# Kernel tuning notes

Measured on AMD Instinct MI355X. Metric: run time of the kernel, lower is better.

## Reference

```python
import jax, jax.numpy as jnp
import numpy as np

N, EG, T, H, EC, L, NT = 10000, 200000, 300000, 128, 128, 3, 100


def _ssp(x):
    # ShiftedSoftplus: softplus(x) - log(2)
    return jax.nn.softplus(x) - jnp.log(2.0).astype(x.dtype)


def _bn(x, g, b):
    # BatchNorm1d in training mode: biased batch stats, eps=1e-5
    m = jnp.mean(x, axis=0)
    v = jnp.var(x, axis=0)
    return g * (x - m) * jax.lax.rsqrt(v + 1e-5) + b


def _forward(z, i, j, idx_i, idx_j, idx_k, idx_ji, idx_kj, pos,
             We1, be1, We2, be2, We3, be3,
             Wc1, bc1, g_c1, b_c1, g_n, b_n,
             Wc2, bc2, g_c2, b_c2, Wc3, bc3, g_c3, b_c3,
             g_c22, b_c22, g_c32, b_c32,
             Wf1, bf1, Wf2, bf2, Wf3, bf3):
    # AtomType2NodeEmb
    h = jax.nn.one_hot(z, NT, dtype=jnp.float32)
    h = _ssp(h @ We1 + be1)
    h = _ssp(h @ We2 + be2)
    node = h @ We3 + be3                      # [N, H]
    # geometry + GaussianFilter edge embedding
    rel = pos[i] - pos[j]                     # [EG, 3]
    dist = jnp.sqrt(jnp.sum(rel * rel, axis=-1))
    unit = rel / dist[:, None]
    offset = jnp.linspace(0.0, 5.0, EC)
    coeff = -0.5 / (offset[1] - offset[0]) ** 2
    edge = jnp.exp(coeff * (dist[:, None] - offset[None, :]) ** 2)  # [EG, EC]
    for l in range(L):
        # NodeUpdate
        c1 = jnp.concatenate([node[i], edge], axis=1) @ Wc1[l] + bc1[l]
        c1 = _bn(c1, g_c1[l], b_c1[l])
        f1, r1 = jnp.split(c1, 2, axis=1)
        agg = jax.ops.segment_sum(jax.nn.sigmoid(f1) * jnp.tanh(r1), i, num_segments=N)
        node = jnp.tanh(node + _bn(agg, g_n[l], b_n[l]))
        # EdgeUpdate: pair term
        c2 = (node[i] * node[j]) @ Wc2[l] + bc2[l]
        c2 = _bn(c2, g_c2[l], b_c2[l])
        f2, r2 = jnp.split(c2, 2, axis=1)
        c2_emb = _bn(jax.nn.sigmoid(f2) * jnp.tanh(r2), g_c22[l], b_c22[l])
        # EdgeUpdate: triplet term
        c3 = jnp.concatenate([node[idx_i], node[idx_j], node[idx_k],
                              edge[idx_ji], edge[idx_kj]], axis=1) @ Wc3[l] + bc3[l]
        c3 = _bn(c3, g_c3[l], b_c3[l])
        f3, r3 = jnp.split(c3, 2, axis=1)
        agg3 = jax.ops.segment_sum(jax.nn.sigmoid(f3) * jnp.tanh(r3), idx_ji, num_segments=EG)
        c3_emb = _bn(agg3, g_c32[l], b_c32[l])
        edge = jnp.tanh(edge + c2_emb + c3_emb)
    # ForcePredictor
    f = _ssp(edge @ Wf1 + bf1)
    f = _ssp(f @ Wf2 + bf2)
    force = (f @ Wf3 + bf3) * unit            # [EG, 3]
    return jax.ops.segment_sum(force, i, num_segments=N)


def setup_inputs() -> dict:
    ks = iter(jax.random.split(jax.random.key(0), 32))

    def w(shape):
        return jax.random.normal(next(ks), shape, jnp.float32) * (shape[-2] ** -0.5)

    z = jax.random.randint(next(ks), (N,), 0, NT)
    pos = jax.random.uniform(next(ks), (N, 3), jnp.float32) * 5.0
    i = jax.random.randint(next(ks), (EG,), 0, N)
    j = (i + 1 + jax.random.randint(next(ks), (EG,), 0, N - 1)) % N  # no self-loops
    idx_i = jax.random.randint(next(ks), (T,), 0, N)
    idx_j = jax.random.randint(next(ks), (T,), 0, N)
    idx_k = jax.random.randint(next(ks), (T,), 0, N)
    idx_ji = jax.random.randint(next(ks), (T,), 0, EG)
    idx_kj = jax.random.randint(next(ks), (T,), 0, EG)
    return dict(
        z=z, pos=pos, i=i, j=j, idx_i=idx_i, idx_j=idx_j, idx_k=idx_k,
        idx_ji=idx_ji, idx_kj=idx_kj,
        We1=w((NT, H)), be1=jnp.zeros((H,)), We2=w((H, H)), be2=jnp.zeros((H,)),
        We3=w((H, H)), be3=jnp.zeros((H,)),
        Wc1=w((L, H + EC, 2 * H)), bc1=jnp.zeros((L, 2 * H)),
        g_c1=jnp.ones((L, 2 * H)), b_c1=jnp.zeros((L, 2 * H)),
        g_n=jnp.ones((L, H)), b_n=jnp.zeros((L, H)),
        Wc2=w((L, H, 2 * EC)), bc2=jnp.zeros((L, 2 * EC)),
        g_c2=jnp.ones((L, 2 * EC)), b_c2=jnp.zeros((L, 2 * EC)),
        Wc3=w((L, 3 * H + 2 * EC, 2 * EC)), bc3=jnp.zeros((L, 2 * EC)),
        g_c3=jnp.ones((L, 2 * EC)), b_c3=jnp.zeros((L, 2 * EC)),
        g_c22=jnp.ones((L, EC)), b_c22=jnp.zeros((L, EC)),
        g_c32=jnp.ones((L, EC)), b_c32=jnp.zeros((L, EC)),
        Wf1=w((EC, EC)), bf1=jnp.zeros((EC,)), Wf2=w((EC, EC)), bf2=jnp.zeros((EC,)),
        Wf3=w((EC, 1)), bf3=jnp.zeros((1,)),
    )


def reference(z, pos, i, j, idx_i, idx_j, idx_k, idx_ji, idx_kj,
              We1, be1, We2, be2, We3, be3,
              Wc1, bc1, g_c1, b_c1, g_n, b_n,
              Wc2, bc2, g_c2, b_c2, Wc3, bc3, g_c3, b_c3,
              g_c22, b_c22, g_c32, b_c32,
              Wf1, bf1, Wf2, bf2, Wf3, bf3):
    return _forward(z, i, j, idx_i, idx_j, idx_k, idx_ji, idx_kj, pos,
                    We1, be1, We2, be2, We3, be3,
                    Wc1, bc1, g_c1, b_c1, g_n, b_n,
                    Wc2, bc2, g_c2, b_c2, Wc3, bc3, g_c3, b_c3,
                    g_c22, b_c22, g_c32, b_c32,
                    Wf1, bf1, Wf2, bf2, Wf3, bf3)
```

## Files before the change

kernel.cpp:

```cpp
#include <hip/hip_runtime.h>

typedef unsigned short u16;
typedef unsigned int   u32;
typedef __attribute__((ext_vector_type(8))) short short8;
typedef __attribute__((ext_vector_type(4))) float f32x4;

#define NN  10000
#define EGN 200000
#define TTN 300000
#define LLN 3

__device__ __forceinline__ float b2f(u16 u){ union{u32 i; float f;} x; x.i=(u32)u<<16; return x.f; }
__device__ __forceinline__ u16 f2b(float f){ union{float f; u32 u;} x; x.f=f; u32 r=(x.u + 0x7fffu + ((x.u>>16)&1u))>>16; return (u16)r; }
__device__ __forceinline__ float sigf(float x){ return 1.f/(1.f+__expf(-x)); }
__device__ __forceinline__ float tanhf_(float x){ float e=__expf(2.f*x); return 1.f - 2.f/(e+1.f); }
__device__ __forceinline__ float sspf(float x){ return fmaxf(x,0.f) + log1pf(__expf(-fabsf(x))) - 0.6931471805599453f; }

__device__ __forceinline__ void async16(void* lds, const void* g){
  __builtin_amdgcn_global_load_lds((const __attribute__((address_space(1))) void*)g,
                                   (__attribute__((address_space(3))) void*)lds, 16, 0, 0);
}
__device__ __forceinline__ void split_store(float v, u16* ph, u16* pl, size_t o){
  u16 h = f2b(v); ph[o] = h; pl[o] = f2b(v - b2f(h));
}
__device__ __forceinline__ short8 ldfrag(const u16* P, int row, int kk, int lane){
  int kg = kk*4 + (lane>>4);
  int slot = kg ^ (row&7);
  return *(const short8*)(P + row*64 + slot*8);
}

struct Segs {
  const u16* sh[10];
  const u16* sl[10];
  const int* idx[10];
  int coff[10];
};

template<int NP, int ROWS>
__device__ __forceinline__ void stageA(u16* Ah, u16* Al,
    const u16* sh, const u16* sl, const int* idxp, int coff,
    int rb, int M, int tid){
#pragma unroll
  for (int rnd=0; rnd<ROWS/32; ++rnd){
    int u = rnd*256 + tid;
    int row = u>>3, s = u&7, sw = s ^ (row&7);
    int grow = rb + row; if (grow >= M) grow = M-1;
    int srow = idxp ? idxp[grow] : grow;
    size_t go = (size_t)srow*256 + coff + sw*16;
    async16(Ah + u*8, (const char*)sh + go);
    if (NP==2) async16(Al + u*8, (const char*)sl + go);
  }
}

template<int NP, int ROWS>
__device__ __forceinline__ void stageA_prod(u16* Ah, u16* Al,
    const u16* nh, const u16* nl, const int* pii, const int* pjj,
    int rb, int M, int ks, int tid){
#pragma unroll
  for (int rep=0; rep<ROWS/64; ++rep){
    int row = rep*64 + (tid>>2), q = tid&3;
    int e = rb + row; if (e >= M) e = M-1;
    int ia = pii[e], ja = pjj[e];
    const u16* phi = nh + (size_t)ia*128 + ks*64 + q*16;
    const u16* pli = nl + (size_t)ia*128 + ks*64 + q*16;
    const u16* phj = nh + (size_t)ja*128 + ks*64 + q*16;
    const u16* plj = nl + (size_t)ja*128 + ks*64 + q*16;
#pragma unroll
    for (int c=0;c<2;c++){
      short8 hi = *(const short8*)(phi + c*8);
      short8 li = *(const short8*)(pli + c*8);
      short8 hj = *(const short8*)(phj + c*8);
      short8 lj = *(const short8*)(plj + c*8);
      short8 vh, vl;
#pragma unroll
      for (int k=0;k<8;k++){
        float a = b2f((u16)hi[k]) + b2f((u16)li[k]);
        float b = b2f((u16)hj[k]) + b2f((u16)lj[k]);
        float v = a*b;
        u16 h = f2b(v);
        vh[k] = (short)h;
        vl[k] = (short)f2b(v - b2f(h));
      }
      int g = q*2 + c, slot = g ^ (row&7);
      *(short8*)(Ah + row*64 + slot*8) = vh;
      if (NP==2) *(short8*)(Al + row*64 + slot*8) = vl;
    }
  }
}

// ... 55 lines not shown
    for (int kk=0;kk<2;kk++){
      short8 a[4];
#pragma unroll
      for (int m=0;m<4;m++) a[m] = ldfrag(Ah, m*16 + lane15, kk, lane);
#pragma unroll
      for (int n=0;n<4;n++){
        short8 b = ldfrag(Bh, wv*64 + n*16 + lane15, kk, lane);
#pragma unroll
        for (int m=0;m<4;m++)
          acc[m][n] = __builtin_amdgcn_mfma_f32_16x16x32_bf16(a[m], b, acc[m][n], 0,0,0);
      }
    }
    __syncthreads();
  }
#pragma unroll
  for (int n=0;n<4;n++){
    int col = wv*64 + n*16 + lane15;
    float bb = bias[col];
    float s=0.f, q=0.f;
#pragma unroll
    for (int m=0;m<4;m++){
#pragma unroll
      for (int r=0;r<4;r++){
        int grow = rb + m*16 + (lane>>4)*4 + r;
        if (grow < M){ float v = acc[m][n][r] + bb; s += v; q += v*v; }
      }
    }
    s += __shfl_xor(s,16); s += __shfl_xor(s,32);
    q += __shfl_xor(q,16); q += __shfl_xor(q,32);
    if (lane < 16){ atomicAdd(&ls[wv*64 + n*16 + lane], s); atomicAdd(&lq[wv*64 + n*16 + lane], q); }
  }
  __syncthreads();
  atomicAdd(&st[tid], ls[tid]); atomicAdd(&st[256+tid], lq[tid]);
}

template<int NP, bool PROD, int EPI>
__global__ __launch_bounds__(256) void gemm_pair(
  int M, int nseg, Segs segs,
  const u16* __restrict__ nh, const u16* __restrict__ nl,
  const int* __restrict__ pii, const int* __restrict__ pjj,
  const u16* __restrict__ Wh, const u16* __restrict__ Wl, int K2b,
  const float* __restrict__ bias,
  const float* __restrict__ st, const float* __restrict__ g, const float* __restrict__ b, float inv,
  const int* __restrict__ sidx, float* __restrict__ aggout,
  const float* __restrict__ st22, const float* __restrict__ g22, const float* __restrict__ b22,
  const float* __restrict__ st32, const float* __restrict__ g32, const float* __restrict__ b32, float inv2,
  const float* __restrict__ agg3, u16* __restrict__ eh, u16* __restrict__ el,
  float* __restrict__ st22out)
{
  __shared__ u16 Ah[64*64];
  __shared__ u16 Al[NP==2 ? 64*64 : 64];
  __shared__ u16 Bh[128*64];
  __shared__ u16 Bl[NP==2 ? 128*64 : 64];
  __shared__ float ls[64], lq[64];
  __shared__ float sAf[64], sCf[64], sAr[64], sCr[64];
  __shared__ float sA22[64], sC22[64], sA32[64], sC32[64];
  const int tid = threadIdx.x, lane = tid&63, wv = tid>>6;
  const int lane15 = lane&15;
  const int rb = blockIdx.x*64, P0 = blockIdx.y*64;

  if (tid < 64){
    int p = P0 + tid;
    float m1 = st[p]*inv,     v1 = st[256+p]*inv - m1*m1;
    float a1 = g[p]*rsqrtf(v1+1e-5f);
    sAf[tid]=a1; sCf[tid]=b[p]-a1*m1;
    float m2 = st[128+p]*inv, v2 = st[384+p]*inv - m2*m2;
    float a2 = g[128+p]*rsqrtf(v2+1e-5f);
    sAr[tid]=a2; sCr[tid]=b[128+p]-a2*m2;
    if (EPI==1){
      float m3 = st22[p]*inv2, v3 = st22[128+p]*inv2 - m3*m3;
      float a3 = g22[p]*rsqrtf(v3+1e-5f);
      sA22[tid]=a3; sC22[tid]=b22[p]-a3*m3;
      float m4 = st32[p]*inv2, v4 = st32[128+p]*inv2 - m4*m4;
      float a4 = g32[p]*rsqrtf(v4+1e-5f);
      sA32[tid]=a4; sC32[tid]=b32[p]-a4*m4;
    }
    if (EPI==2){ ls[tid]=0.f; lq[tid]=0.f; }
  }

  f32x4 accf[4], accr[4];
#pragma unroll
  for (int m=0;m<4;m++){ accf[m]=(f32x4){0.f,0.f,0.f,0.f}; accr[m]=(f32x4){0.f,0.f,0.f,0.f}; }

  for (int ks=0; ks<nseg; ++ks){
    if (PROD) stageA_prod<NP,64>(Ah, Al, nh, nl, pii, pjj, rb, M, ks, tid);
    else      stageA<NP,64>(Ah, Al, segs.sh[ks], segs.sl[ks], segs.idx[ks], segs.coff[ks], rb, M, tid);
    stageB_pair<NP>(Bh, Bl, Wh, Wl, P0, K2b, ks*128, tid);
    __syncthreads();
#pragma unroll
    for (int kk=0;kk<2;kk++){
      short8 ah[4], al[4];
#pragma unroll
      for (int m=0;m<4;m++){
        ah[m] = ldfrag(Ah, m*16 + lane15, kk, lane);
        if constexpr (NP==2) al[m] = ldfrag(Al, m*16 + lane15, kk, lane);
      }
      short8 bfh = ldfrag(Bh, wv*16 + lane15,      kk, lane);
      short8 brh = ldfrag(Bh, 64 + wv*16 + lane15, kk, lane);
      short8 bfl, brl;
      if constexpr (NP==2){
        bfl = ldfrag(Bl, wv*16 + lane15,      kk, lane);
        brl = ldfrag(Bl, 64 + wv*16 + lane15, kk, lane);
      }
#pragma unroll
      for (int m=0;m<4;m++){
        accf[m] = __builtin_amdgcn_mfma_f32_16x16x32_bf16(ah[m], bfh, accf[m], 0,0,0);
        accr[m] = __builtin_amdgcn_mfma_f32_16x16x32_bf16(ah[m], brh, accr[m], 0,0,0);
        if constexpr (NP==2){
          accf[m] = __builtin_amdgcn_mfma_f32_16x16x32_bf16(ah[m], bfl, accf[m], 0,0,0);
          accf[m] = __builtin_amdgcn_mfma_f32_16x16x32_bf16(al[m], bfh, accf[m], 0,0,0);
          accr[m] = __builtin_amdgcn_mfma_f32_16x16x32_bf16(ah[m], brl, accr[m], 0,0,0);
          accr[m] = __builtin_amdgcn_mfma_f32_16x16x32_bf16(al[m], brh, accr[m], 0,0,0);
        }
      }
    }
    __syncthreads();
  }

  const int pp = wv*16 + lane15;
  const int p  = P0 + pp;
  const float bf_ = bias[p], br_ = bias[128+p];
  const float Af = sAf[pp], Cf = sCf[pp], Ar = sAr[pp], Cr = sCr[pp];
  float su=0.f, sq=0.f;
#pragma unroll
  for (int m=0;m<4;m++){
#pragma unroll
    for (int r=0;r<4;r++){
      int grow = rb + m*16 + (lane>>4)*4 + r;
      if (grow >= M) continue;
      float yf = accf[m][r] + bf_;
      float yr = accr[m][r] + br_;
      float u = sigf(Af*yf + Cf) * tanhf_(Ar*yr + Cr);
      if (EPI==0){
        atomicAdd(&aggout[(size_t)sidx[grow]*128 + p], u);
      } else if (EPI==1){
        size_t o = (size_t)grow*128 + p;
        float eo = b2f(eh[o]) + b2f(el[o]);
        float v = tanhf_(eo + sA22[pp]*u + sC22[pp] + sA32[pp]*agg3[o] + sC32[pp]);
        split_store(v, eh, el, o);
      } else {
        su += u; sq += u*u;
      }
    }
  }
  if (EPI==2){
    su += __shfl_xor(su,16); su += __shfl_xor(su,32);
    sq += __shfl_xor(sq,16); sq += __shfl_xor(sq,32);
    if (lane < 16){ atomicAdd(&ls[wv*16+lane], su); atomicAdd(&lq[wv*16+lane], sq); }
    __syncthreads();
    if (tid < 64){ atomicAdd(&st22out[P0+tid], ls[tid]); atomicAdd(&st22out[128+P0+tid], lq[tid]); }
  }
}

__global__ __launch_bounds__(256) void gemm_force(
  int M, Segs segs,
  const u16* __restrict__ Wh, const u16* __restrict__ Wl, int K2b,
  const float* __restrict__ bias, u16* __restrict__ oh, u16* __restrict__ ol)
{
  __shared__ u16 Ah[64*64], Al[64*64];
  __shared__ u16 Bh[128*64], Bl[128*64];
  const int tid = threadIdx.x, lane = tid&63, wv = tid>>6;
  const int lane15 = lane&15;
  const int rb = blockIdx.x*64;

  f32x4 acc[4][2];
#pragma unroll
  for (int m=0;m<4;m++)
#pragma unroll
    for (int n=0;n<2;n++) acc[m][n] = (f32x4){0.f,0.f,0.f,0.f};

  for (int ks=0; ks<2; ++ks){
    stageA<2,64>(Ah, Al, segs.sh[ks], segs.sl[ks], segs.idx[ks], segs.coff[ks], rb, M, tid);
    stageB_id<2,128>(Bh, Bl, Wh, Wl, K2b, ks*128, tid);
    __syncthreads();
#pragma unroll
    for (int kk=0;kk<2;kk++){
      short8 ah[4], al[4];
#pragma unroll
      for (int m=0;m<4;m++){
        ah[m] = ldfrag(Ah, m*16 + lane15, kk, lane);
        al[m] = ldfrag(Al, m*16 + lane15, kk, lane);
      }
#pragma unroll
      for (int n=0;n<2;n++){
        short8 bh = ldfrag(Bh, wv*32 + n*16 + lane15, kk, lane);
        short8 bl = ldfrag(Bl, wv*32 + n*16 + lane15, kk, lane);
#pragma unroll
        for (int m=0;m<4;m++){
          acc[m][n] = __builtin_amdgcn_mfma_f32_16x16x32_bf16(ah[m], bh, acc[m][n], 0,0,0);
          acc[m][n] = __builtin_amdgcn_mfma_f32_16x16x32_bf16(ah[m], bl, acc[m][n], 0,0,0);
          acc[m][n] = __builtin_amdgcn_mfma_f32_16x16x32_bf16(al[m], bh, acc[m][n], 0,0,0);
        }
      }
    }
    __syncthreads();
  }
#pragma unroll
  for (int n=0;n<2;n++){
    int col = wv*32 + n*16 + lane15;
    float bb = bias[col];
#pragma unroll
    for (int m=0;m<4;m++){
#pragma unroll
      for (int r=0;r<4;r++){
        int grow = rb + m*16 + (lane>>4)*4 + r;
        if (grow < M){
          float v = sspf(acc[m][n][r] + bb);
          split_store(v, oh, ol, (size_t)grow*128 + col);
        }
      }
    }
  }
}

__global__ void transpose_cvt(const float* __restrict__ src, u16* __restrict__ dh, u16* __restrict__ dl, int K, int N){
  __shared__ float t[32][33];
  const float* s = src + (size_t)blockIdx.z * K * N;
  u16* dsth = dh + (size_t)blockIdx.z * K * N;
  u16* dstl = dl + (size_t)blockIdx.z * K * N;
  int n0 = blockIdx.x*32, k0 = blockIdx.y*32;
  for (int dy=threadIdx.y; dy<32; dy+=8){
    int k = k0+dy, n = n0+threadIdx.x;
    if (k<K && n<N) t[dy][threadIdx.x] = s[(size_t)k*N + n];
  }
  __syncthreads();
  for (int dy=threadIdx.y; dy<32; dy+=8){
    int n = n0+dy, k = k0+threadIdx.x;
    if (n<N && k<K) split_store(t[threadIdx.x][dy], dsth, dstl, (size_t)n*K + k);
  }
}

__global__ __launch_bounds__(128) void embed_k(const int* __restrict__ z,
  const float* __restrict__ We1, const float* __restrict__ be1,
  const float* __restrict__ We2, const float* __restrict__ be2,
  const float* __restrict__ We3, const float* __restrict__ be3,
  u16* __restrict__ nh, u16* __restrict__ nl){
  __shared__ float h0[128], h1[128];
  int nid = blockIdx.x, t = threadIdx.x;
  int zz = z[nid];
  h0[t] = sspf(We1[zz*128 + t] + be1[t]);
  __syncthreads();
  float a = be2[t];
  for (int k=0;k<128;k++) a += h0[k]*We2[k*128+t];
  h1[t] = sspf(a);
  __syncthreads();
  float b = be3[t];
  for (int k=0;k<128;k++) b += h1[k]*We3[k*128+t];
  split_store(b, nh, nl, (size_t)nid*128+t);
}

__global__ __launch_bounds__(256) void geom_k(const float* __restrict__ pos,
  const int* __restrict__ ii, const int* __restrict__ jj,
  float* __restrict__ unitv, u16* __restrict__ eh, u16* __restrict__ el){
  int t = threadIdx.x; int e = blockIdx.x*2 + (t>>7); int col = t&127;
  int a = ii[e], b = jj[e];
  float dx = pos[a*3]-pos[b*3], dy=pos[a*3+1]-pos[b*3+1], dz=pos[a*3+2]-pos[b*3+2];
  float dist = sqrtf(dx*dx+dy*dy+dz*dz);
  if (col==0){ float inv=1.f/dist; unitv[e*3]=dx*inv; unitv[e*3+1]=dy*inv; unitv[e*3+2]=dz*inv; }
  const float step = 5.0f/127.0f;
  const float coeff = -0.5f/(step*step);
  float d = dist - step*(float)col;
  float g = __expf(coeff*d*d);
  split_store(g, eh, el, (size_t)e*128+col);
}

__global__ __launch_bounds__(256) void colstats128(const float* __restrict__ m, int M, float* __restrict__ st){
  __shared__ float ls[128], lq[128];
  int t=threadIdx.x; if(t<128){ls[t]=0.f;lq[t]=0.f;} __syncthreads();
  int col=t&127, hf=t>>7; float ps=0.f,pq=0.f;
  int npair=(M+1)>>1;
  for (int pr=blockIdx.x; pr<npair; pr+=gridDim.x){
    int row=pr*2+hf;
    if(row<M){ float v=m[(size_t)row*128+col]; ps+=v; pq+=v*v; }
  }
  atomicAdd(&ls[col],ps); atomicAdd(&lq[col],pq);
  __syncthreads();
  if(t<128){ atomicAdd(&st[t],ls[t]); atomicAdd(&st[128+t],lq[t]); }
}

__global__ __launch_bounds__(256) void node_update_k(u16* __restrict__ nh, u16* __restrict__ nl,
  const float* __restrict__ agg, const float* __restrict__ st,
  const float* __restrict__ g, const float* __restrict__ b, float inv, int Nn)
{
  int t=threadIdx.x; int col=t&127, hf=t>>7;
  float mean = st[col]*inv;
  float var  = st[128+col]*inv - mean*mean;
  float A = g[col]*rsqrtf(var+1e-5f);
  float C = b[col] - A*mean;
  int npair=(Nn+1)>>1;
  for (int pr=blockIdx.x; pr<npair; pr+=gridDim.x){
    int row=pr*2+hf; if(row>=Nn) continue;
    size_t o=(size_t)row*128+col;
    float nv = b2f(nh[o]) + b2f(nl[o]);
    float v = tanhf_(nv + A*agg[o] + C);
    split_store(v, nh, nl, o);
  }
}

__global__ __launch_bounds__(256) void force_k(const u16* __restrict__ fh, const u16* __restrict__ fl,
  const float* __restrict__ Wf3, const float* __restrict__ bf3,
  const float* __restrict__ unitv, const int* __restrict__ ii, float* __restrict__ outp, int Me)
{
  int wv=threadIdx.x>>6, lane=threadIdx.x&63;
  int e = blockIdx.x*4 + wv; if(e>=Me) return;
  size_t o0=(size_t)e*128+lane, o1=o0+64;
  float p = (b2f(fh[o0])+b2f(fl[o0]))*Wf3[lane] + (b2f(fh[o1])+b2f(fl[o1]))*Wf3[64+lane];
  for (int s=32;s>0;s>>=1) p += __shfl_down(p, s);
  if (lane==0){
    float F = p + bf3[0];
    atomicAdd(&outp[ii[e]*3+0], F*unitv[e*3+0]);
    atomicAdd(&outp[ii[e]*3+1], F*unitv[e*3+1]);
    atomicAdd(&outp[ii[e]*3+2], F*unitv[e*3+2]);
  }
}

__global__ void sentinel_k(float* o, int n, float v){
  int i = blockIdx.x*256 + threadIdx.x; if (i<n) o[i]=v;
}

extern "C" void kernel_launch(void* const* d_in, const int* in_sizes, int n_in,
                              void* d_out, int out_size, void* d_ws, size_t ws_size,
                              hipStream_t stream)
{
  (void)in_sizes; (void)n_in;
  const int* z      = (const int*)d_in[0];
  const float* pos  = (const float*)d_in[1];
  const int* ii     = (const int*)d_in[2];
  const int* jj     = (const int*)d_in[3];
  const int* idx_i  = (const int*)d_in[4];
  const int* idx_j  = (const int*)d_in[5];
  const int* idx_k  = (const int*)d_in[6];
  const int* idx_ji = (const int*)d_in[7];
  const int* idx_kj = (const int*)d_in[8];
  const float* We1=(const float*)d_in[9];  const float* be1=(const float*)d_in[10];
  const float* We2=(const float*)d_in[11]; const float* be2=(const float*)d_in[12];
  const float* We3=(const float*)d_in[13]; const float* be3=(const float*)d_in[14];
  const float* Wc1=(const float*)d_in[15]; const float* bc1=(const float*)d_in[16];
  const float* g_c1=(const float*)d_in[17]; const float* b_c1=(const float*)d_in[18];
  const float* g_n=(const float*)d_in[19]; const float* b_n=(const float*)d_in[20];
  const float* Wc2=(const float*)d_in[21]; const float* bc2=(const float*)d_in[22];
  const float* g_c2=(const float*)d_in[23]; const float* b_c2=(const float*)d_in[24];
  const float* Wc3=(const float*)d_in[25]; const float* bc3=(const float*)d_in[26];
  const float* g_c3=(const float*)d_in[27]; const float* b_c3=(const float*)d_in[28];
  const float* g_c22=(const float*)d_in[29]; const float* b_c22=(const float*)d_in[30];
  const float* g_c32=(const float*)d_in[31]; const float* b_c32=(const float*)d_in[32];
  const float* Wf1=(const float*)d_in[33]; const float* bf1=(const float*)d_in[34];
  const float* Wf2=(const float*)d_in[35]; const float* bf2=(const float*)d_in[36];
  const float* Wf3=(const float*)d_in[37]; const float* bf3=(const float*)d_in[38];

  char* ws = (char*)d_ws;
  size_t off=0;
  auto alloc=[&](size_t bb){ size_t o=off; off += (bb+255)&~(size_t)255; return o; };
  u16*   node_h = (u16*)(ws + alloc((size_t)NN*128*2));
  u16*   node_l = (u16*)(ws + alloc((size_t)NN*128*2));
  u16*   edge_h = (u16*)(ws + alloc((size_t)EGN*128*2));
  u16*   edge_l = (u16*)(ws + alloc((size_t)EGN*128*2));
  float* unitv  = (float*)(ws + alloc((size_t)EGN*3*4));
  float* agg    = (float*)(ws + alloc((size_t)NN*128*4));
  float* agg3   = (float*)(ws + alloc((size_t)EGN*128*4));
  u16*   wc1h   = (u16*)(ws + alloc((size_t)3*256*256*2));
  u16*   wc1l   = (u16*)(ws + alloc((size_t)3*256*256*2));
  u16*   wc2h   = (u16*)(ws + alloc((size_t)3*256*128*2));
  u16*   wc2l   = (u16*)(ws + alloc((size_t)3*256*128*2));
  u16*   wc3h   = (u16*)(ws + alloc((size_t)3*256*640*2));
  u16*   wc3l   = (u16*)(ws + alloc((size_t)3*256*640*2));
  u16*   wf1h   = (u16*)(ws + alloc((size_t)128*128*2));
  u16*   wf1l   = (u16*)(ws + alloc((size_t)128*128*2));
  u16*   wf2h   = (u16*)(ws + alloc((size_t)128*128*2));
  u16*   wf2l   = (u16*)(ws + alloc((size_t)128*128*2));
  float* stats  = (float*)(ws + alloc(2304*4));

  if (off > ws_size){
    sentinel_k<<<(out_size+255)/256, 256, 0, stream>>>((float*)d_out, out_size, 123456.0f);
    return;
  }

  float* st1 = stats;
  float* st2 = stats+512;
  float* st3 = stats+1024;
  float* stN = stats+1536;
  float* st32= stats+1792;
  float* st22= stats+2048;

  u16* f1h = (u16*)agg3;
  u16* f1l = f1h + (size_t)EGN*128;
  u16* f2h = edge_h;
  u16* f2l = edge_l;

  hipMemsetAsync(d_out, 0, (size_t)out_size*4, stream);

  dim3 tb(32,8);
  transpose_cvt<<<dim3(8,8,3),  tb, 0, stream>>>(Wc1, wc1h, wc1l, 256, 256);
  transpose_cvt<<<dim3(8,4,3),  tb, 0, stream>>>(Wc2, wc2h, wc2l, 128, 256);
  transpose_cvt<<<dim3(8,20,3), tb, 0, stream>>>(Wc3, wc3h, wc3l, 640, 256);
  transpose_cvt<<<dim3(4,4,1),  tb, 0, stream>>>(Wf1, wf1h, wf1l, 128, 128);
  transpose_cvt<<<dim3(4,4,1),  tb, 0, stream>>>(Wf2, wf2h, wf2l, 128, 128);

  embed_k<<<NN,128,0,stream>>>(z, We1,be1,We2,be2,We3,be3, node_h, node_l);
  geom_k<<<EGN/2,256,0,stream>>>(pos, ii, jj, unitv, edge_h, edge_l);

  const int gE64  = (EGN+63)/64;
  const int gT64  = (TTN+63)/64;
  Segs dummy{};
  const float invE = 1.0f/EGN, invT = 1.0f/TTN, invN = 1.0f/NN;

  for (int l=0;l<LLN;l++){
    hipMemsetAsync(stats, 0, 2304*4, stream);
    hipMemsetAsync(agg,  0, (size_t)NN*128*4, stream);
    hipMemsetAsync(agg3, 0, (size_t)EGN*128*4, stream);

    const u16* w1h = wc1h + l*256*256; const u16* w1l = wc1l + l*256*256;
    const u16* w2h = wc2h + l*256*128; const u16* w2l = wc2l + l*256*128;
    const u16* w3h = wc3h + l*256*640; const u16* w3l = wc3l + l*256*640;

    Segs s1{};
    s1.sh[0]=node_h; s1.sl[0]=node_l; s1.idx[0]=ii;      s1.coff[0]=0;
    s1.sh[1]=node_h; s1.sl[1]=node_l; s1.idx[1]=ii;      s1.coff[1]=128;
    s1.sh[2]=edge_h; s1.sl[2]=edge_l; s1.idx[2]=nullptr; s1.coff[2]=0;
    s1.sh[3]=edge_h; s1.sl[3]=edge_l; s1.idx[3]=nullptr; s1.coff[3]=128;
    gemm_stats<false><<<gE64,256,0,stream>>>(EGN, 4, s1, nullptr,nullptr,nullptr,nullptr,
                                             w1h, 512, bc1+l*256, st1);
    gemm_pair<2,false,0><<<dim3(gE64,2),256,0,stream>>>(EGN, 4, s1, nullptr,nullptr,nullptr,nullptr,
        w1h, w1l, 512, bc1+l*256,
        st1, g_c1+l*256, b_c1+l*256, invE,
        ii, agg,
        nullptr,nullptr,nullptr, nullptr,nullptr,nullptr, 0.f,
        nullptr, nullptr, nullptr, nullptr);
    colstats128<<<256,256,0,stream>>>(agg, NN, stN);
    node_update_k<<<2048,256,0,stream>>>(node_h, node_l, agg, stN, g_n+l*128, b_n+l*128, invN, NN);

    Segs s3{};
    s3.sh[0]=node_h; s3.sl[0]=node_l; s3.idx[0]=idx_i;  s3.coff[0]=0;
    s3.sh[1]=node_h; s3.sl[1]=node_l; s3.idx[1]=idx_i;  s3.coff[1]=128;
    s3.sh[2]=node_h; s3.sl[2]=node_l; s3.idx[2]=idx_j;  s3.coff[2]=0;
    s3.sh[3]=node_h; s3.sl[3]=node_l; s3.idx[3]=idx_j;  s3.coff[3]=128;
    s3.sh[4]=node_h; s3.sl[4]=node_l; s3.idx[4]=idx_k;  s3.coff[4]=0;
    s3.sh[5]=node_h; s3.sl[5]=node_l; s3.idx[5]=idx_k;  s3.coff[5]=128;
    s3.sh[6]=edge_h; s3.sl[6]=edge_l; s3.idx[6]=idx_ji; s3.coff[6]=0;
    s3.sh[7]=edge_h; s3.sl[7]=edge_l; s3.idx[7]=idx_ji; s3.coff[7]=128;
    s3.sh[8]=edge_h; s3.sl[8]=edge_l; s3.idx[8]=idx_kj; s3.coff[8]=0;
    s3.sh[9]=edge_h; s3.sl[9]=edge_l; s3.idx[9]=idx_kj; s3.coff[9]=128;
    gemm_stats<false><<<gT64,256,0,stream>>>(TTN, 10, s3, nullptr,nullptr,nullptr,nullptr,
                                             w3h, 1280, bc3+l*256, st3);
    gemm_pair<2,false,0><<<dim3(gT64,2),256,0,stream>>>(TTN, 10, s3, nullptr,nullptr,nullptr,nullptr,
        w3h, w3l, 1280, bc3+l*256,
        st3, g_c3+l*256, b_c3+l*256, invT,
        idx_ji, agg3,
        nullptr,nullptr,nullptr, nullptr,nullptr,nullptr, 0.f,
        nullptr, nullptr, nullptr, nullptr);
    colstats128<<<1024,256,0,stream>>>(agg3, EGN, st32);

    gemm_stats<true><<<gE64,256,0,stream>>>(EGN, 2, dummy, node_h,node_l,ii,jj,
                                            w2h, 256, bc2+l*256, st2);
    gemm_pair<1,true,2><<<dim3(gE64,2),256,0,stream>>>(EGN, 2, dummy, node_h,node_l,ii,jj,
        w2h, nullptr, 256, bc2+l*256,
        st2, g_c2+l*256, b_c2+l*256, invE,
        nullptr, nullptr,
        nullptr,nullptr,nullptr, nullptr,nullptr,nullptr, 0.f,
        nullptr, nullptr, nullptr, st22);
    gemm_pair<2,true,1><<<dim3(gE64,2),256,0,stream>>>(EGN, 2, dummy, node_h,node_l,ii,jj,
        w2h, w2l, 256, bc2+l*256,
        st2, g_c2+l*256, b_c2+l*256, invE,
        nullptr, nullptr,
        st22, g_c22+l*128, b_c22+l*128, st32, g_c32+l*128, b_c32+l*128, invE,
        agg3, edge_h, edge_l, nullptr);
  }

  Segs sf1{}; sf1.sh[0]=edge_h; sf1.sl[0]=edge_l; sf1.idx[0]=nullptr; sf1.coff[0]=0;
              sf1.sh[1]=edge_h; sf1.sl[1]=edge_l; sf1.idx[1]=nullptr; sf1.coff[1]=128;
  gemm_force<<<gE64,256,0,stream>>>(EGN, sf1, wf1h, wf1l, 256, bf1, f1h, f1l);
  Segs sf2{}; sf2.sh[0]=f1h; sf2.sl[0]=f1l; sf2.idx[0]=nullptr; sf2.coff[0]=0;
              sf2.sh[1]=f1h; sf2.sl[1]=f1l; sf2.idx[1]=nullptr; sf2.coff[1]=128;
  gemm_force<<<gE64,256,0,stream>>>(EGN, sf2, wf2h, wf2l, 256, bf2, f2h, f2l);
  force_k<<<(EGN+3)/4,256,0,stream>>>(f2h, f2l, Wf3, bf3, unitv, ii, (float*)d_out, EGN);
}
```

Before: 4.164 ms.

## Sort edges and triplets by scatter key and coalesce segment-sum atomics

Adds a per-call counting sort (histogram, scan, rank, permute) that reorders edges by source node and triplets by their remapped target edge. All edge state is stored in sorted order and the triplet indices are remapped to match. The EPI==0 epilogue then accumulates consecutive rows that share a segment id in registers and issues one atomic per run instead of one per row. This is meant to cut global atomic traffic and improve gather locality, at the cost of about twenty extra small launches and nondeterministic ordering within each segment from the atomic-based ranking.

```diff
diff --git a/kernel.cpp b/kernel.cpp
--- a/kernel.cpp
+++ b/kernel.cpp
@@ -35,6 +35,61 @@
   const int* idx[10];
   int coff[10];
 };
+
+__global__ void hist_k(const int* __restrict__ keys, int n, int* __restrict__ hist){
+  int i = blockIdx.x*256 + threadIdx.x;
+  if (i<n) atomicAdd(&hist[keys[i]], 1);
+}
+__global__ __launch_bounds__(256) void scan_tile_k(const int* __restrict__ in, int n,
+                                                   int* __restrict__ out, int* __restrict__ tilesum){
+  __shared__ int ts[256];
+  int b=blockIdx.x, t=threadIdx.x;
+  int base=b*2048+t*8;
+  int v[8], s=0;
+#pragma unroll
+  for(int k=0;k<8;k++){ int i=base+k; v[k]=(i<n)?in[i]:0; s+=v[k]; }
+  ts[t]=s; __syncthreads();
+  if(t==0){ int acc=0; for(int k=0;k<256;k++){int x=ts[k]; ts[k]=acc; acc+=x;} tilesum[b]=acc; }
+  __syncthreads();
+  int acc=ts[t];
+#pragma unroll
+  for(int k=0;k<8;k++){ int i=base+k; if(i<n) out[i]=acc; acc+=v[k]; }
+}
+__global__ void scan_sum_k(int* tilesum, int ntiles){
+  if(threadIdx.x==0 && blockIdx.x==0){
+    int acc=0; for(int k=0;k<ntiles;k++){int x=tilesum[k]; tilesum[k]=acc; acc+=x;}
+  }
+}
+__global__ __launch_bounds__(256) void scan_add_k(int* __restrict__ out, int n, const int* __restrict__ tilesum){
+  int i=blockIdx.x*256+threadIdx.x; if(i<n) out[i] += tilesum[i>>11];
+}
+__global__ void rank_k(const int* __restrict__ keys, int n, const int* __restrict__ basearr,
+                       int* __restrict__ cnt, int* __restrict__ rank){
+  int i=blockIdx.x*256+threadIdx.x; if(i>=n) return;
+  int k=keys[i];
+  rank[i] = basearr[k] + atomicAdd(&cnt[k],1);
+}
+__global__ void remap2_k(const int* __restrict__ a, const int* __restrict__ b,
+                         const int* __restrict__ table, int n,
+                         int* __restrict__ oa, int* __restrict__ ob){
+  int i=blockIdx.x*256+threadIdx.x; if(i>=n) return;
+  oa[i]=table[a[i]]; ob[i]=table[b[i]];
+}
+__global__ void permute2_k(const int* __restrict__ rank, int n,
+                           const int* __restrict__ a, const int* __restrict__ b,
+                           int* __restrict__ pa, int* __restrict__ pb){
+  int i=blockIdx.x*256+threadIdx.x; if(i>=n) return;
+  int r=rank[i]; pa[r]=a[i]; pb[r]=b[i];
+}
+__global__ void permute5_k(const int* __restrict__ rank, int n,
+                           const int* __restrict__ a, const int* __restrict__ b, const int* __restrict__ c,
+                           const int* __restrict__ d, const int* __restrict__ e,
+                           int* __restrict__ pa, int* __restrict__ pb, int* __restrict__ pc,
+                           int* __restrict__ pd, int* __restrict__ pe){
+  int i=blockIdx.x*256+threadIdx.x; if(i>=n) return;
+  int r=rank[i];
+  pa[r]=a[i]; pb[r]=b[i]; pc[r]=c[i]; pd[r]=d[i]; pe[r]=e[i];
+}
 
 template<int NP, int ROWS>
 __device__ __forceinline__ void stageA(u16* Ah, u16* Al,
@@ -265,34 +320,55 @@
   const int p  = P0 + pp;
   const float bf_ = bias[p], br_ = bias[128+p];
   const float Af = sAf[pp], Cf = sCf[pp], Ar = sAr[pp], Cr = sCr[pp];
-  float su=0.f, sq=0.f;
-#pragma unroll
-  for (int m=0;m<4;m++){
-#pragma unroll
-    for (int r=0;r<4;r++){
-      int grow = rb + m*16 + (lane>>4)*4 + r;
-      if (grow >= M) continue;
-      float yf = accf[m][r] + bf_;
-      float yr = accr[m][r] + br_;
-      float u = sigf(Af*yf + Cf) * tanhf_(Ar*yr + Cr);
-      if (EPI==0){
-        atomicAdd(&aggout[(size_t)sidx[grow]*128 + p], u);
-      } else if (EPI==1){
-        size_t o = (size_t)grow*128 + p;
-        float eo = b2f(eh[o]) + b2f(el[o]);
-        float v = tanhf_(eo + sA22[pp]*u + sC22[pp] + sA32[pp]*agg3[o] + sC32[pp]);
-        split_store(v, eh, el, o);
-      } else {
-        su += u; sq += u*u;
-      }
-    }
-  }
-  if (EPI==2){
-    su += __shfl_xor(su,16); su += __shfl_xor(su,32);
-    sq += __shfl_xor(sq,16); sq += __shfl_xor(sq,32);
-    if (lane < 16){ atomicAdd(&ls[wv*16+lane], su); atomicAdd(&lq[wv*16+lane], sq); }
-    __syncthreads();
-    if (tid < 64){ atomicAdd(&st22out[P0+tid], ls[tid]); atomicAdd(&st22out[128+P0+tid], lq[tid]); }
+
+  if constexpr (EPI==0){
+    int cur = -1; float run = 0.f;
+#pragma unroll
+    for (int m=0;m<4;m++){
+#pragma unroll
+      for (int r=0;r<4;r++){
+        int grow = rb + m*16 + (lane>>4)*4 + r;
+        if (grow >= M) continue;
+        float yf = accf[m][r] + bf_;
+        float yr = accr[m][r] + br_;
+        float u = sigf(Af*yf + Cf) * tanhf_(Ar*yr + Cr);
+        int sv = sidx[grow];
+        if (sv != cur){
+          if (cur >= 0) atomicAdd(&aggout[(size_t)cur*128 + p], run);
+          cur = sv; run = 0.f;
+        }
+        run += u;
+      }
+    }
+    if (cur >= 0) atomicAdd(&aggout[(size_t)cur*128 + p], run);
+  } else {
+    float su=0.f, sq=0.f;
+#pragma unroll
+    for (int m=0;m<4;m++){
+#pragma unroll
+      for (int r=0;r<4;r++){
+        int grow = rb + m*16 + (lane>>4)*4 + r;
+        if (grow >= M) continue;
+        float yf = accf[m][r] + bf_;
+        float yr = accr[m][r] + br_;
+        float u = sigf(Af*yf + Cf) * tanhf_(Ar*yr + Cr);
+        if (EPI==1){
+          size_t o = (size_t)grow*128 + p;
+          float eo = b2f(eh[o]) + b2f(el[o]);
+          float v = tanhf_(eo + sA22[pp]*u + sC22[pp] + sA32[pp]*agg3[o] + sC32[pp]);
+          split_store(v, eh, el, o);
+        } else {
+          su += u; sq += u*u;
+        }
+      }
+    }
+    if (EPI==2){
+      su += __shfl_xor(su,16); su += __shfl_xor(su,32);
+      sq += __shfl_xor(sq,16); sq += __shfl_xor(sq,32);
+      if (lane < 16){ atomicAdd(&ls[wv*16+lane], su); atomicAdd(&lq[wv*16+lane], sq); }
+      __syncthreads();
+      if (tid < 64){ atomicAdd(&st22out[P0+tid], ls[tid]); atomicAdd(&st22out[128+P0+tid], lq[tid]); }
+    }
   }
 }
 
@@ -394,18 +470,19 @@
 }
 
 __global__ __launch_bounds__(256) void geom_k(const float* __restrict__ pos,
-  const int* __restrict__ ii, const int* __restrict__ jj,
+  const int* __restrict__ ii, const int* __restrict__ jj, const int* __restrict__ ranke,
   float* __restrict__ unitv, u16* __restrict__ eh, u16* __restrict__ el){
   int t = threadIdx.x; int e = blockIdx.x*2 + (t>>7); int col = t&127;
   int a = ii[e], b = jj[e];
+  int r = ranke[e];
   float dx = pos[a*3]-pos[b*3], dy=pos[a*3+1]-pos[b*3+1], dz=pos[a*3+2]-pos[b*3+2];
   float dist = sqrtf(dx*dx+dy*dy+dz*dz);
-  if (col==0){ float inv=1.f/dist; unitv[e*3]=dx*inv; unitv[e*3+1]=dy*inv; unitv[e*3+2]=dz*inv; }
+  if (col==0){ float inv=1.f/dist; unitv[r*3]=dx*inv; unitv[r*3+1]=dy*inv; unitv[r*3+2]=dz*inv; }
   const float step = 5.0f/127.0f;
   const float coeff = -0.5f/(step*step);
   float d = dist - step*(float)col;
   float g = __expf(coeff*d*d);
-  split_store(g, eh, el, (size_t)e*128+col);
+  split_store(g, eh, el, (size_t)r*128+col);
 }
 
 __global__ __launch_bounds__(256) void colstats128(const float* __restrict__ m, int M, float* __restrict__ st){
@@ -443,7 +520,7 @@
 
 __global__ __launch_bounds__(256) void force_k(const u16* __restrict__ fh, const u16* __restrict__ fl,
   const float* __restrict__ Wf3, const float* __restrict__ bf3,
-  const float* __restrict__ unitv, const int* __restrict__ ii, float* __restrict__ outp, int Me)
+  const float* __restrict__ unitv, const int* __restrict__ pii, float* __restrict__ outp, int Me)
 {
   int wv=threadIdx.x>>6, lane=threadIdx.x&63;
   int e = blockIdx.x*4 + wv; if(e>=Me) return;
@@ -452,9 +529,9 @@
   for (int s=32;s>0;s>>=1) p += __shfl_down(p, s);
   if (lane==0){
     float F = p + bf3[0];
-    atomicAdd(&outp[ii[e]*3+0], F*unitv[e*3+0]);
-    atomicAdd(&outp[ii[e]*3+1], F*unitv[e*3+1]);
-    atomicAdd(&outp[ii[e]*3+2], F*unitv[e*3+2]);
+    atomicAdd(&outp[pii[e]*3+0], F*unitv[e*3+0]);
+    atomicAdd(&outp[pii[e]*3+1], F*unitv[e*3+1]);
+    atomicAdd(&outp[pii[e]*3+2], F*unitv[e*3+2]);
   }
 }
 
@@ -513,6 +590,21 @@
   u16*   wf2h   = (u16*)(ws + alloc((size_t)128*128*2));
   u16*   wf2l   = (u16*)(ws + alloc((size_t)128*128*2));
   float* stats  = (float*)(ws + alloc(2304*4));
+  int* rank_e  = (int*)(ws + alloc((size_t)EGN*4));
+  int* pii     = (int*)(ws + alloc((size_t)EGN*4));
+  int* pjj     = (int*)(ws + alloc((size_t)EGN*4));
+  int* rji     = (int*)(ws + alloc((size_t)TTN*4));
+  int* rkj     = (int*)(ws + alloc((size_t)TTN*4));
+  int* rank_t  = (int*)(ws + alloc((size_t)TTN*4));
+  int* pidx_i  = (int*)(ws + alloc((size_t)TTN*4));
+  int* pidx_j  = (int*)(ws + alloc((size_t)TTN*4));
+  int* pidx_k  = (int*)(ws + alloc((size_t)TTN*4));
+  int* pidx_ji = (int*)(ws + alloc((size_t)TTN*4));
+  int* pidx_kj = (int*)(ws + alloc((size_t)TTN*4));
+  int* hist    = (int*)(ws + alloc((size_t)EGN*4));
+  int* ebase   = (int*)(ws + alloc((size_t)EGN*4));
+  int* cnt     = (int*)(ws + alloc((size_t)EGN*4));
+  int* tilesum = (int*)(ws + alloc(128*4));
 
   if (off > ws_size){
     sentinel_k<<<(out_size+255)/256, 256, 0, stream>>>((float*)d_out, out_size, 123456.0f);
@@ -533,6 +625,26 @@
 
   hipMemsetAsync(d_out, 0, (size_t)out_size*4, stream);
 
+  hipMemsetAsync(hist, 0, NN*4, stream);
+  hist_k<<<(EGN+255)/256,256,0,stream>>>(ii, EGN, hist);
+  scan_tile_k<<<(NN+2047)/2048,256,0,stream>>>(hist, NN, ebase, tilesum);
+  scan_sum_k<<<1,64,0,stream>>>(tilesum, (NN+2047)/2048);
+  scan_add_k<<<(NN+255)/256,256,0,stream>>>(ebase, NN, tilesum);
+  hipMemsetAsync(cnt, 0, NN*4, stream);
+  rank_k<<<(EGN+255)/256,256,0,stream>>>(ii, EGN, ebase, cnt, rank_e);
+  permute2_k<<<(EGN+255)/256,256,0,stream>>>(rank_e, EGN, ii, jj, pii, pjj);
+
+  remap2_k<<<(TTN+255)/256,256,0,stream>>>(idx_ji, idx_kj, rank_e, TTN, rji, rkj);
+  hipMemsetAsync(hist, 0, (size_t)EGN*4, stream);
+  hist_k<<<(TTN+255)/256,256,0,stream>>>(rji, TTN, hist);
+  scan_tile_k<<<(EGN+2047)/2048,256,0,stream>>>(hist, EGN, ebase, tilesum);
+  scan_sum_k<<<1,64,0,stream>>>(tilesum, (EGN+2047)/2048);
+  scan_add_k<<<(EGN+255)/256,256,0,stream>>>(ebase, EGN, tilesum);
+  hipMemsetAsync(cnt, 0, (size_t)EGN*4, stream);
+  rank_k<<<(TTN+255)/256,256,0,stream>>>(rji, TTN, ebase, cnt, rank_t);
+  permute5_k<<<(TTN+255)/256,256,0,stream>>>(rank_t, TTN, idx_i, idx_j, idx_k, rji, rkj,
+                                             pidx_i, pidx_j, pidx_k, pidx_ji, pidx_kj);
+
   dim3 tb(32,8);
   transpose_cvt<<<dim3(8,8,3),  tb, 0, stream>>>(Wc1, wc1h, wc1l, 256, 256);
   transpose_cvt<<<dim3(8,4,3),  tb, 0, stream>>>(Wc2, wc2h, wc2l, 128, 256);
@@ -541,7 +653,7 @@
   transpose_cvt<<<dim3(4,4,1),  tb, 0, stream>>>(Wf2, wf2h, wf2l, 128, 128);
 
   embed_k<<<NN,128,0,stream>>>(z, We1,be1,We2,be2,We3,be3, node_h, node_l);
-  geom_k<<<EGN/2,256,0,stream>>>(pos, ii, jj, unitv, edge_h, edge_l);
+  geom_k<<<EGN/2,256,0,stream>>>(pos, ii, jj, rank_e, unitv, edge_h, edge_l);
 
   const int gE64  = (EGN+63)/64;
   const int gT64  = (TTN+63)/64;
@@ -558,8 +670,8 @@
     const u16* w3h = wc3h + l*256*640; const u16* w3l = wc3l + l*256*640;
 
     Segs s1{};
-    s1.sh[0]=node_h; s1.sl[0]=node_l; s1.idx[0]=ii;      s1.coff[0]=0;
-    s1.sh[1]=node_h; s1.sl[1]=node_l; s1.idx[1]=ii;      s1.coff[1]=128;
+    s1.sh[0]=node_h; s1.sl[0]=node_l; s1.idx[0]=pii;     s1.coff[0]=0;
+    s1.sh[1]=node_h; s1.sl[1]=node_l; s1.idx[1]=pii;     s1.coff[1]=128;
     s1.sh[2]=edge_h; s1.sl[2]=edge_l; s1.idx[2]=nullptr; s1.coff[2]=0;
     s1.sh[3]=edge_h; s1.sl[3]=edge_l; s1.idx[3]=nullptr; s1.coff[3]=128;
     gemm_stats<false><<<gE64,256,0,stream>>>(EGN, 4, s1, nullptr,nullptr,nullptr,nullptr,
@@ -567,42 +679,42 @@
     gemm_pair<2,false,0><<<dim3(gE64,2),256,0,stream>>>(EGN, 4, s1, nullptr,nullptr,nullptr,nullptr,
         w1h, w1l, 512, bc1+l*256,
         st1, g_c1+l*256, b_c1+l*256, invE,
-        ii, agg,
+        pii, agg,
         nullptr,nullptr,nullptr, nullptr,nullptr,nullptr, 0.f,
         nullptr, nullptr, nullptr, nullptr);
     colstats128<<<256,256,0,stream>>>(agg, NN, stN);
     node_update_k<<<2048,256,0,stream>>>(node_h, node_l, agg, stN, g_n+l*128, b_n+l*128, invN, NN);
 
     Segs s3{};
-    s3.sh[0]=node_h; s3.sl[0]=node_l; s3.idx[0]=idx_i;  s3.coff[0]=0;
-    s3.sh[1]=node_h; s3.sl[1]=node_l; s3.idx[1]=idx_i;  s3.coff[1]=128;
-    s3.sh[2]=node_h; s3.sl[2]=node_l; s3.idx[2]=idx_j;  s3.coff[2]=0;
-    s3.sh[3]=node_h; s3.sl[3]=node_l; s3.idx[3]=idx_j;  s3.coff[3]=128;
-    s3.sh[4]=node_h; s3.sl[4]=node_l; s3.idx[4]=idx_k;  s3.coff[4]=0;
-    s3.sh[5]=node_h; s3.sl[5]=node_l; s3.idx[5]=idx_k;  s3.coff[5]=128;
-    s3.sh[6]=edge_h; s3.sl[6]=edge_l; s3.idx[6]=idx_ji; s3.coff[6]=0;
-    s3.sh[7]=edge_h; s3.sl[7]=edge_l; s3.idx[7]=idx_ji; s3.coff[7]=128;
-    s3.sh[8]=edge_h; s3.sl[8]=edge_l; s3.idx[8]=idx_kj; s3.coff[8]=0;
-    s3.sh[9]=edge_h; s3.sl[9]=edge_l; s3.idx[9]=idx_kj; s3.coff[9]=128;
+    s3.sh[0]=node_h; s3.sl[0]=node_l; s3.idx[0]=pidx_i;  s3.coff[0]=0;
+    s3.sh[1]=node_h; s3.sl[1]=node_l; s3.idx[1]=pidx_i;  s3.coff[1]=128;
+    s3.sh[2]=node_h; s3.sl[2]=node_l; s3.idx[2]=pidx_j;  s3.coff[2]=0;
+    s3.sh[3]=node_h; s3.sl[3]=node_l; s3.idx[3]=pidx_j;  s3.coff[3]=128;
+    s3.sh[4]=node_h; s3.sl[4]=node_l; s3.idx[4]=pidx_k;  s3.coff[4]=0;
+    s3.sh[5]=node_h; s3.sl[5]=node_l; s3.idx[5]=pidx_k;  s3.coff[5]=128;
+    s3.sh[6]=edge_h; s3.sl[6]=edge_l; s3.idx[6]=pidx_ji; s3.coff[6]=0;
+    s3.sh[7]=edge_h; s3.sl[7]=edge_l; s3.idx[7]=pidx_ji; s3.coff[7]=128;
+    s3.sh[8]=edge_h; s3.sl[8]=edge_l; s3.idx[8]=pidx_kj; s3.coff[8]=0;
+    s3.sh[9]=edge_h; s3.sl[9]=edge_l; s3.idx[9]=pidx_kj; s3.coff[9]=128;
     gemm_stats<false><<<gT64,256,0,stream>>>(TTN, 10, s3, nullptr,nullptr,nullptr,nullptr,
                                              w3h, 1280, bc3+l*256, st3);
     gemm_pair<2,false,0><<<dim3(gT64,2),256,0,stream>>>(TTN, 10, s3, nullptr,nullptr,nullptr,nullptr,
         w3h, w3l, 1280, bc3+l*256,
         st3, g_c3+l*256, b_c3+l*256, invT,
-        idx_ji, agg3,
+        pidx_ji, agg3,
         nullptr,nullptr,nullptr, nullptr,nullptr,nullptr, 0.f,
         nullptr, nullptr, nullptr, nullptr);
     colstats128<<<1024,256,0,stream>>>(agg3, EGN, st32);
 
-    gemm_stats<true><<<gE64,256,0,stream>>>(EGN, 2, dummy, node_h,node_l,ii,jj,
+    gemm_stats<true><<<gE64,256,0,stream>>>(EGN, 2, dummy, node_h,node_l,pii,pjj,
                                             w2h, 256, bc2+l*256, st2);
-    gemm_pair<1,true,2><<<dim3(gE64,2),256,0,stream>>>(EGN, 2, dummy, node_h,node_l,ii,jj,
+    gemm_pair<1,true,2><<<dim3(gE64,2),256,0,stream>>>(EGN, 2, dummy, node_h,node_l,pii,pjj,
         w2h, nullptr, 256, bc2+l*256,
         st2, g_c2+l*256, b_c2+l*256, invE,
         nullptr, nullptr,
         nullptr,nullptr,nullptr, nullptr,nullptr,nullptr, 0.f,
         nullptr, nullptr, nullptr, st22);
-    gemm_pair<2,true,1><<<dim3(gE64,2),256,0,stream>>>(EGN, 2, dummy, node_h,node_l,ii,jj,
+    gemm_pair<2,true,1><<<dim3(gE64,2),256,0,stream>>>(EGN, 2, dummy, node_h,node_l,pii,pjj,
         w2h, w2l, 256, bc2+l*256,
         st2, g_c2+l*256, b_c2+l*256, invE,
         nullptr, nullptr,
@@ -616,5 +728,5 @@
   Segs sf2{}; sf2.sh[0]=f1h; sf2.sl[0]=f1l; sf2.idx[0]=nullptr; sf2.coff[0]=0;
               sf2.sh[1]=f1h; sf2.sl[1]=f1l; sf2.idx[1]=nullptr; sf2.coff[1]=128;
   gemm_force<<<gE64,256,0,stream>>>(EGN, sf2, wf2h, wf2l, 256, bf2, f2h, f2l);
-  force_k<<<(EGN+3)/4,256,0,stream>>>(f2h, f2l, Wf3, bf3, unitv, ii, (float*)d_out, EGN);
-}
+  force_k<<<(EGN+3)/4,256,0,stream>>>(f2h, f2l, Wf3, bf3, unitv, pii, (float*)d_out, EGN);
+}
```

New measurement: 4.223 ms. No clear change (+1.4%).

## Cover all output columns per block in gemm_pair to reuse gathered A tile

Applied to the files above, without the earlier changes.

gemm_pair previously launched two column-half blocks per row tile, each re-gathering the same indexed A rows from node/edge arrays. Now one block loops over both column halves and keeps twice the accumulators, staging B per half while reusing the A tile already in LDS. This halves the gather traffic and the grid size, but doubles accumulator registers (possible occupancy loss) and adds extra barriers per segment.

```diff
diff --git a/kernel.cpp b/kernel.cpp
--- a/kernel.cpp
+++ b/kernel.cpp
@@ -196,15 +196,16 @@
   __shared__ u16 Al[NP==2 ? 64*64 : 64];
   __shared__ u16 Bh[128*64];
   __shared__ u16 Bl[NP==2 ? 128*64 : 64];
-  __shared__ float ls[64], lq[64];
-  __shared__ float sAf[64], sCf[64], sAr[64], sCr[64];
-  __shared__ float sA22[64], sC22[64], sA32[64], sC32[64];
+  __shared__ float ls[EPI==2 ? 128 : 1], lq[EPI==2 ? 128 : 1];
+  __shared__ float sAf[128], sCf[128], sAr[128], sCr[128];
+  __shared__ float sA22[EPI==1 ? 128 : 1], sC22[EPI==1 ? 128 : 1];
+  __shared__ float sA32[EPI==1 ? 128 : 1], sC32[EPI==1 ? 128 : 1];
   const int tid = threadIdx.x, lane = tid&63, wv = tid>>6;
   const int lane15 = lane&15;
-  const int rb = blockIdx.x*64, P0 = blockIdx.y*64;
-
-  if (tid < 64){
-    int p = P0 + tid;
+  const int rb = blockIdx.x*64;
+
+  if (tid < 128){
+    int p = tid;
     float m1 = st[p]*inv,     v1 = st[256+p]*inv - m1*m1;
     float a1 = g[p]*rsqrtf(v1+1e-5f);
     sAf[tid]=a1; sCf[tid]=b[p]-a1*m1;
@@ -222,77 +223,86 @@
     if (EPI==2){ ls[tid]=0.f; lq[tid]=0.f; }
   }
 
-  f32x4 accf[4], accr[4];
-#pragma unroll
-  for (int m=0;m<4;m++){ accf[m]=(f32x4){0.f,0.f,0.f,0.f}; accr[m]=(f32x4){0.f,0.f,0.f,0.f}; }
+  f32x4 accf[2][4], accr[2][4];
+#pragma unroll
+  for (int h=0;h<2;h++)
+#pragma unroll
+    for (int m=0;m<4;m++){ accf[h][m]=(f32x4){0.f,0.f,0.f,0.f}; accr[h][m]=(f32x4){0.f,0.f,0.f,0.f}; }
 
   for (int ks=0; ks<nseg; ++ks){
     if (PROD) stageA_prod<NP,64>(Ah, Al, nh, nl, pii, pjj, rb, M, ks, tid);
     else      stageA<NP,64>(Ah, Al, segs.sh[ks], segs.sl[ks], segs.idx[ks], segs.coff[ks], rb, M, tid);
-    stageB_pair<NP>(Bh, Bl, Wh, Wl, P0, K2b, ks*128, tid);
+#pragma unroll
+    for (int h=0;h<2;h++){
+      stageB_pair<NP>(Bh, Bl, Wh, Wl, h*64, K2b, ks*128, tid);
+      __syncthreads();
+#pragma unroll
+      for (int kk=0;kk<2;kk++){
+        short8 ah[4], al[4];
+#pragma unroll
+        for (int m=0;m<4;m++){
+          ah[m] = ldfrag(Ah, m*16 + lane15, kk, lane);
+          if constexpr (NP==2) al[m] = ldfrag(Al, m*16 + lane15, kk, lane);
+        }
+        short8 bfh = ldfrag(Bh, wv*16 + lane15,      kk, lane);
+        short8 brh = ldfrag(Bh, 64 + wv*16 + lane15, kk, lane);
+        short8 bfl, brl;
+        if constexpr (NP==2){
+          bfl = ldfrag(Bl, wv*16 + lane15,      kk, lane);
+          brl = ldfrag(Bl, 64 + wv*16 + lane15, kk, lane);
+        }
+#pragma unroll
+        for (int m=0;m<4;m++){
+          accf[h][m] = __builtin_amdgcn_mfma_f32_16x16x32_bf16(ah[m], bfh, accf[h][m], 0,0,0);
+          accr[h][m] = __builtin_amdgcn_mfma_f32_16x16x32_bf16(ah[m], brh, accr[h][m], 0,0,0);
+          if constexpr (NP==2){
+            accf[h][m] = __builtin_amdgcn_mfma_f32_16x16x32_bf16(ah[m], bfl, accf[h][m], 0,0,0);
+            accf[h][m] = __builtin_amdgcn_mfma_f32_16x16x32_bf16(al[m], bfh, accf[h][m], 0,0,0);
+            accr[h][m] = __builtin_amdgcn_mfma_f32_16x16x32_bf16(ah[m], brl, accr[h][m], 0,0,0);
+            accr[h][m] = __builtin_amdgcn_mfma_f32_16x16x32_bf16(al[m], brh, accr[h][m], 0,0,0);
+          }
+        }
+      }
+      __syncthreads();
+    }
+  }
+
+#pragma unroll
+  for (int h=0;h<2;h++){
+    const int pp = h*64 + wv*16 + lane15;
+    const float bf_ = bias[pp], br_ = bias[128+pp];
+    const float Af = sAf[pp], Cf = sCf[pp], Ar = sAr[pp], Cr = sCr[pp];
+    float su=0.f, sq=0.f;
+#pragma unroll
+    for (int m=0;m<4;m++){
+#pragma unroll
+      for (int r=0;r<4;r++){
+        int grow = rb + m*16 + (lane>>4)*4 + r;
+        if (grow >= M) continue;
+        float yf = accf[h][m][r] + bf_;
+        float yr = accr[h][m][r] + br_;
+        float u = sigf(Af*yf + Cf) * tanhf_(Ar*yr + Cr);
+        if (EPI==0){
+          atomicAdd(&aggout[(size_t)sidx[grow]*128 + pp], u);
+        } else if (EPI==1){
+          size_t o = (size_t)grow*128 + pp;
+          float eo = b2f(eh[o]) + b2f(el[o]);
+          float v = tanhf_(eo + sA22[pp]*u + sC22[pp] + sA32[pp]*agg3[o] + sC32[pp]);
+          split_store(v, eh, el, o);
+        } else {
+          su += u; sq += u*u;
+        }
+      }
+    }
+    if (EPI==2){
+      su += __shfl_xor(su,16); su += __shfl_xor(su,32);
+      sq += __shfl_xor(sq,16); sq += __shfl_xor(sq,32);
+      if (lane < 16){ atomicAdd(&ls[h*64 + wv*16 + lane], su); atomicAdd(&lq[h*64 + wv*16 + lane], sq); }
+    }
+  }
+  if (EPI==2){
     __syncthreads();
-#pragma unroll
-    for (int kk=0;kk<2;kk++){
-      short8 ah[4], al[4];
-#pragma unroll
-      for (int m=0;m<4;m++){
-        ah[m] = ldfrag(Ah, m*16 + lane15, kk, lane);
-        if constexpr (NP==2) al[m] = ldfrag(Al, m*16 + lane15, kk, lane);
-      }
-      short8 bfh = ldfrag(Bh, wv*16 + lane15,      kk, lane);
-      short8 brh = ldfrag(Bh, 64 + wv*16 + lane15, kk, lane);
-      short8 bfl, brl;
-      if constexpr (NP==2){
-        bfl = ldfrag(Bl, wv*16 + lane15,      kk, lane);
-        brl = ldfrag(Bl, 64 + wv*16 + lane15, kk, lane);
-      }
-#pragma unroll
-      for (int m=0;m<4;m++){
-        accf[m] = __builtin_amdgcn_mfma_f32_16x16x32_bf16(ah[m], bfh, accf[m], 0,0,0);
-        accr[m] = __builtin_amdgcn_mfma_f32_16x16x32_bf16(ah[m], brh, accr[m], 0,0,0);
-        if constexpr (NP==2){
-          accf[m] = __builtin_amdgcn_mfma_f32_16x16x32_bf16(ah[m], bfl, accf[m], 0,0,0);
-          accf[m] = __builtin_amdgcn_mfma_f32_16x16x32_bf16(al[m], bfh, accf[m], 0,0,0);
-          accr[m] = __builtin_amdgcn_mfma_f32_16x16x32_bf16(ah[m], brl, accr[m], 0,0,0);
-          accr[m] = __builtin_amdgcn_mfma_f32_16x16x32_bf16(al[m], brh, accr[m], 0,0,0);
-        }
-      }
-    }
-    __syncthreads();
-  }
-
-  const int pp = wv*16 + lane15;
-  const int p  = P0 + pp;
-  const float bf_ = bias[p], br_ = bias[128+p];
-  const float Af = sAf[pp], Cf = sCf[pp], Ar = sAr[pp], Cr = sCr[pp];
-  float su=0.f, sq=0.f;
-#pragma unroll
-  for (int m=0;m<4;m++){
-#pragma unroll
-    for (int r=0;r<4;r++){
-      int grow = rb + m*16 + (lane>>4)*4 + r;
-      if (grow >= M) continue;
-      float yf = accf[m][r] + bf_;
-      float yr = accr[m][r] + br_;
-      float u = sigf(Af*yf + Cf) * tanhf_(Ar*yr + Cr);
-      if (EPI==0){
-        atomicAdd(&aggout[(size_t)sidx[grow]*128 + p], u);
-      } else if (EPI==1){
-        size_t o = (size_t)grow*128 + p;
-        float eo = b2f(eh[o]) + b2f(el[o]);
-        float v = tanhf_(eo + sA22[pp]*u + sC22[pp] + sA32[pp]*agg3[o] + sC32[pp]);
-        split_store(v, eh, el, o);
-      } else {
-        su += u; sq += u*u;
-      }
-    }
-  }
-  if (EPI==2){
-    su += __shfl_xor(su,16); su += __shfl_xor(su,32);
-    sq += __shfl_xor(sq,16); sq += __shfl_xor(sq,32);
-    if (lane < 16){ atomicAdd(&ls[wv*16+lane], su); atomicAdd(&lq[wv*16+lane], sq); }
-    __syncthreads();
-    if (tid < 64){ atomicAdd(&st22out[P0+tid], ls[tid]); atomicAdd(&st22out[128+P0+tid], lq[tid]); }
+    if (tid < 128){ atomicAdd(&st22out[tid], ls[tid]); atomicAdd(&st22out[128+tid], lq[tid]); }
   }
 }
 
@@ -564,7 +574,7 @@
     s1.sh[3]=edge_h; s1.sl[3]=edge_l; s1.idx[3]=nullptr; s1.coff[3]=128;
     gemm_stats<false><<<gE64,256,0,stream>>>(EGN, 4, s1, nullptr,nullptr,nullptr,nullptr,
                                              w1h, 512, bc1+l*256, st1);
-    gemm_pair<2,false,0><<<dim3(gE64,2),256,0,stream>>>(EGN, 4, s1, nullptr,nullptr,nullptr,nullptr,
+    gemm_pair<2,false,0><<<gE64,256,0,stream>>>(EGN, 4, s1, nullptr,nullptr,nullptr,nullptr,
         w1h, w1l, 512, bc1+l*256,
         st1, g_c1+l*256, b_c1+l*256, invE,
         ii, agg,
@@ -586,7 +596,7 @@
     s3.sh[9]=edge_h; s3.sl[9]=edge_l; s3.idx[9]=idx_kj; s3.coff[9]=128;
     gemm_stats<false><<<gT64,256,0,stream>>>(TTN, 10, s3, nullptr,nullptr,nullptr,nullptr,
                                              w3h, 1280, bc3+l*256, st3);
-    gemm_pair<2,false,0><<<dim3(gT64,2),256,0,stream>>>(TTN, 10, s3, nullptr,nullptr,nullptr,nullptr,
+    gemm_pair<2,false,0><<<gT64,256,0,stream>>>(TTN, 10, s3, nullptr,nullptr,nullptr,nullptr,
         w3h, w3l, 1280, bc3+l*256,
         st3, g_c3+l*256, b_c3+l*256, invT,
         idx_ji, agg3,
@@ -596,13 +606,13 @@
 
     gemm_stats<true><<<gE64,256,0,stream>>>(EGN, 2, dummy, node_h,node_l,ii,jj,
                                             w2h, 256, bc2+l*256, st2);
-    gemm_pair<1,true,2><<<dim3(gE64,2),256,0,stream>>>(EGN, 2, dummy, node_h,node_l,ii,jj,
+    gemm_pair<1,true,2><<<gE64,256,0,stream>>>(EGN, 2, dummy, node_h,node_l,ii,jj,
         w2h, nullptr, 256, bc2+l*256,
         st2, g_c2+l*256, b_c2+l*256, invE,
         nullptr, nullptr,
         nullptr,nullptr,nullptr, nullptr,nullptr,nullptr, 0.f,
         nullptr, nullptr, nullptr, st22);
-    gemm_pair<2,true,1><<<dim3(gE64,2),256,0,stream>>>(EGN, 2, dummy, node_h,node_l,ii,jj,
+    gemm_pair<2,true,1><<<gE64,256,0,stream>>>(EGN, 2, dummy, node_h,node_l,ii,jj,
         w2h, w2l, 256, bc2+l*256,
         st2, g_c2+l*256, b_c2+l*256, invE,
         nullptr, nullptr,
```

Measured after the change: 4.016 ms, median of 2. -3.6%, faster.
